# Optimization experiments

Hardware: AMD Instinct MI355X
Metric: run time of the kernel (lower is better)

Reference implementation:

```python
import jax, jax.numpy as jnp
import numpy as np

NUM_CLASSES = 2
IGNORE_INDEX = 0
B, H, W = 4, 512, 512
BIG_I = 2 ** 30  # int sentinel for 'no seed yet'
INF = jnp.float32(1e9)  # distance when a column/image has no seed


def _edt_to_seed(seed):
    """Exact 2D Euclidean distance transform: distance from every pixel to the
    nearest True pixel in `seed` [H, W] (matches scipy distance_transform_edt
    applied to an image whose zeros are `seed`).
    Pass 1: 1D nearest-seed distance down each column via cummax/cummin scans.
    Pass 2: exact lower envelope across rows by brute-force min over k:
            D^2(i,j) = min_k ( (j-k)^2 + g(i,k)^2 ).
    """
    h, w = seed.shape
    rows = jnp.arange(h, dtype=jnp.int32)[:, None]              # [H,1]
    last = jax.lax.cummax(jnp.where(seed, rows, -1), axis=0)     # last seed above
    d_fwd = jnp.where(last >= 0, rows - last, BIG_I)
    nxt = jax.lax.cummin(jnp.where(seed, rows, BIG_I), axis=0, reverse=True)
    d_bwd = jnp.where(nxt < BIG_I, nxt - rows, BIG_I)
    g = jnp.minimum(d_fwd, d_bwd)                                # [H,W] int
    g2 = jnp.where(g >= BIG_I // 2, INF * INF, (g * g).astype(jnp.float32))
    cols = jnp.arange(w, dtype=jnp.float32)
    sq = (cols[:, None] - cols[None, :]) ** 2                    # [Wj,Wk]
    d2 = jnp.min(g2[:, None, :] + sq[None, :, :], axis=-1)       # [H,Wj]
    return jnp.sqrt(d2)


def _distance_map_one(tgt):
    """tgt: [H, W] int labels -> [num_classes, H, W] signed distance maps."""
    maps = []
    for c in range(NUM_CLASSES):
        if c == IGNORE_INDEX:
            maps.append(jnp.zeros(tgt.shape, jnp.float32))
            continue
        mask = tgt == c
        pos_dist = _edt_to_seed(~mask)   # edt(posmask): dist to nearest background
        neg_dist = _edt_to_seed(mask)    # edt(negmask): dist to nearest foreground
        present = jnp.any(mask)          # 'if mask.sum() > 0' guard
        maps.append(jnp.where(present, neg_dist - pos_dist, 0.0))
    return jnp.stack(maps, axis=0)


def setup_inputs() -> dict:
    key = jax.random.key(0)
    k1, k2 = jax.random.split(key)
    pred = jax.random.normal(k1, (B, NUM_CLASSES, H, W), dtype=jnp.float32)
    target = jax.random.randint(k2, (B, H, W), 0, 2, dtype=jnp.int32)
    return {"pred": pred, "target": target}


def reference(pred, target):
    p = jax.nn.softmax(pred, axis=1)                         # [B,C,H,W]
    # sequential over batch to bound the [H,W,W] EDT intermediate
    dmaps = jax.lax.map(_distance_map_one, target)           # [B,C,H,W]
    return jnp.mean(p * dmaps)
```

## Files before the change

kernel.cpp:

```cpp
#include <hip/hip_runtime.h>
#include <math.h>

#define BB 4
#define HH 512
#define WW 512
#define HWSZ (HH * WW)
#define ROWS_BLOCKS 256

#define SK(x) ((x) + ((x) >> 5))


__global__ __launch_bounds__(256) void pack_kernel(
    const int* __restrict__ target,
    unsigned int* __restrict__ cw,
    int* __restrict__ flags)
{
    __shared__ int sCnt;
    int gid = blockIdx.x * 256 + threadIdx.x;
    int b = gid >> 13;
    int rem = gid & 8191;
    int w = rem >> 9;
    int col = rem & 511;

    const int* t = target + b * HWSZ + (w << 5) * WW + col;
    unsigned int word = 0;
#pragma unroll
    for (int i = 0; i < 32; ++i)
        word |= (unsigned int)(t[i * WW] == 1) << i;
    cw[gid] = word;

    int cnt = __popc(word);
#pragma unroll
    for (int off = 32; off > 0; off >>= 1) cnt += __shfl_down(cnt, off, 64);
    if (threadIdx.x == 0) sCnt = 0;
    __syncthreads();
    if ((threadIdx.x & 63) == 0) atomicAdd(&sCnt, cnt);
    __syncthreads();
    if (threadIdx.x == 0) flags[blockIdx.x] = (sCnt > 0);
}

__global__ __launch_bounds__(512) void rows_kernel(
    const unsigned int* __restrict__ cw,
    const float* __restrict__ pred,
    float* __restrict__ partials)
{
    __shared__ unsigned int sW[16 * 512];
    __shared__ float g2n[8][SK(511) + 1], g2p[8][SK(511) + 1];

    int blk = blockIdx.x;
    int b = blk >> 6;
    int g = blk & 63;
    int tid = threadIdx.x;
    int w = tid >> 6, lane = tid & 63;
    int row = 8 * g + w;
    int j0 = 8 * lane;

    const float* p0 = pred + (b * 2 + 0) * HWSZ + row * WW + j0;
    const float* p1 = pred + (b * 2 + 1) * HWSZ + row * WW + j0;
    float4 a0 = *(const float4*)(p0);
    float4 a1 = *(const float4*)(p0 + 4);
    float4 c0 = *(const float4*)(p1);
    float4 c1 = *(const float4*)(p1 + 4);

    const unsigned int* cwb = cw + b * 8192;
#pragma unroll
    for (int t = 0; t < 16; ++t)
        sW[tid + 512 * t] = cwb[tid + 512 * t];
    __syncthreads();

    int wr = row >> 5, bit = row & 31;
    float* G2N = g2n[w];
    float* G2P = g2p[w];
    unsigned int loMask = 0xFFFFFFFFu >> (31 - bit);
    unsigned int hiMask = 0xFFFFFFFFu << bit;
#pragma unroll
    for (int t = 0; t < 8; ++t) {
        int col = lane + (t << 6);
        unsigned int Wr = sW[(wr << 9) + col];
        int dUp, dDn;
        unsigned int m = Wr & loMask;
        if (m) dUp = bit - (31 - __builtin_clz(m));
        else {
            dUp = 0x7FFFFFFF;
            for (int q = wr - 1; q >= 0; --q) {
                unsigned int W = sW[(q << 9) + col];
                if (W) { dUp = row - ((q << 5) + 31 - __builtin_clz(W)); break; }
            }
        }
        m = Wr & hiMask;
        if (m) dDn = __builtin_ctz(m) - bit;
        else {
            dDn = 0x7FFFFFFF;
            for (int q = wr + 1; q < 16; ++q) {
                unsigned int W = sW[(q << 9) + col];
                if (W) { dDn = (q << 5) + __builtin_ctz(W) - row; break; }
            }
        }
        int gN = min(dUp, dDn);
        G2N[SK(col)] = (gN > 511) ? 1e18f : (float)(gN * gN);
        unsigned int Vr = ~Wr;
        m = Vr & loMask;
        if (m) dUp = bit - (31 - __builtin_clz(m));
        else {
            dUp = 0x7FFFFFFF;
            for (int q = wr - 1; q >= 0; --q) {
                unsigned int W = ~sW[(q << 9) + col];
                if (W) { dUp = row - ((q << 5) + 31 - __builtin_clz(W)); break; }
            }
        }
        m = Vr & hiMask;
        if (m) dDn = __builtin_ctz(m) - bit;
        else {
            dDn = 0x7FFFFFFF;
            for (int q = wr + 1; q < 16; ++q) {
                unsigned int W = ~sW[(q << 9) + col];
                if (W) { dDn = (q << 5) + __builtin_ctz(W) - row; break; }
            }
        }
        int gP = min(dUp, dDn);
        G2P[SK(col)] = (gP > 511) ? 1e18f : (float)(gP * gP);
    }

    const float* sel[8];
    float bs[8], sgn[8];
#pragma unroll
    for (int jj = 0; jj < 8; ++jj) {
        float on = G2N[SK(j0 + jj)];
        float op = G2P[SK(j0 + jj)];
        bool fg = (on == 0.0f);
        sel[jj] = fg ? G2P : G2N;
        bs[jj]  = fg ? op : on;
        sgn[jj] = fg ? -1.0f : 1.0f;
    }
    for (int r = 1; r < WW; ++r) {
        float sq = (float)(r * r);
        float mx = 0.0f;
#pragma unroll
        for (int jj = 0; jj < 8; ++jj) mx = fmaxf(mx, bs[jj]);
        if (sq >= mx) break;
#pragma unroll
        for (int jj = 0; jj < 8; ++jj) {
            int kl = j0 + jj - r; kl = kl < 0 ? 0 : kl;
            int kr = j0 + jj + r; kr = kr > (WW - 1) ? (WW - 1) : kr;
            bs[jj] = fminf(bs[jj], sq + sel[jj][SK(kl)]);
            bs[jj] = fminf(bs[jj], sq + sel[jj][SK(kr)]);
        }
    }

    float x0[8] = {a0.x, a0.y, a0.z, a0.w, a1.x, a1.y, a1.z, a1.w};
    float x1[8] = {c0.x, c0.y, c0.z, c0.w, c1.x, c1.y, c1.z, c1.w};
    float acc = 0.0f;
#pragma unroll
    for (int jj = 0; jj < 8; ++jj) {
        float dist = sgn[jj] * sqrtf(bs[jj]);
        float prob = 1.0f / (1.0f + __expf(x0[jj] - x1[jj]));
        acc += prob * dist;
    }
#pragma unroll
    for (int off = 32; off > 0; off >>= 1) acc += __shfl_down(acc, off, 64);
    if (lane == 0) partials[b * HH + row] = acc;
}

__global__ __launch_bounds__(64) void finalize_kernel(
    const int* __restrict__ flags,
    const float* __restrict__ partials,
    float* __restrict__ out)
{
    int k = threadIdx.x;

    double presd[BB];
#pragma unroll
    for (int b = 0; b < BB; ++b) {
        int f = (k < 32) ? flags[b * 32 + k] : 0;
        presd[b] = (__ballot(f != 0) != 0ULL) ? 1.0 : 0.0;
    }

    const float4* p4 = (const float4*)partials;
    double s = 0.0;
#pragma unroll
    for (int t = 0; t < 8; ++t) {
        int v4 = k + 64 * t;
        float4 v = p4[v4];
        double gd = presd[v4 >> 7];
        s += gd * ((double)v.x + (double)v.y + (double)v.z + (double)v.w);
    }
#pragma unroll
    for (int off = 32; off > 0; off >>= 1) s += __shfl_down(s, off, 64);
    if (k == 0)
        out[0] = (float)(s * (1.0 / 2097152.0));
}

extern "C" void kernel_launch(void* const* d_in, const int* in_sizes, int n_in,
                              void* d_out, int out_size, void* d_ws, size_t ws_size,
                              hipStream_t stream) {
    const float* pred = (const float*)d_in[0];
    const int* target = (const int*)d_in[1];
    float* out = (float*)d_out;

    char* ws = (char*)d_ws;
    int* flags = (int*)(ws + 0);
    float* partials = (float*)(ws + 1024);
    unsigned int* cw = (unsigned int*)(ws + 32768);

    pack_kernel<<<128, 256, 0, stream>>>(target, cw, flags);
    rows_kernel<<<ROWS_BLOCKS, 512, 0, stream>>>(cw, pred, partials);
    finalize_kernel<<<1, 64, 0, stream>>>(flags, partials, out);
}
```

Measured before the change: 72.45 us.

## Fuse finalize into rows kernel via atomic last-block reduction; vectorize pack

Drops the separate finalize kernel. Each rows block now reduces its warp sums, atomically adds them into a global double accumulator when its batch has a foreground pixel, and the last block to finish writes the mean. The pack kernel now handles four columns per thread with int4 loads and uint4 stores, using 32 blocks instead of 128. The rows kernel copies the packed words into shared memory as uint4. This removes one launch and the partials round trip, at the cost of global atomics and a summation order that is no longer deterministic.

```diff
diff --git a/kernel.cpp b/kernel.cpp
--- a/kernel.cpp
+++ b/kernel.cpp
@@ -13,23 +13,32 @@
 __global__ __launch_bounds__(256) void pack_kernel(
     const int* __restrict__ target,
     unsigned int* __restrict__ cw,
-    int* __restrict__ flags)
+    int* __restrict__ flags,
+    double* __restrict__ dacc,
+    unsigned int* __restrict__ done)
 {
     __shared__ int sCnt;
-    int gid = blockIdx.x * 256 + threadIdx.x;
-    int b = gid >> 13;
-    int rem = gid & 8191;
-    int w = rem >> 9;
-    int col = rem & 511;
+    int q = blockIdx.x * 256 + threadIdx.x;
+    int b = q >> 11;
+    int rem = q & 2047;
+    int w = rem >> 7;
+    int col = (rem & 127) << 2;
+
+    if (q == 0) { *dacc = 0.0; *done = 0u; }
 
     const int* t = target + b * HWSZ + (w << 5) * WW + col;
-    unsigned int word = 0;
-#pragma unroll
-    for (int i = 0; i < 32; ++i)
-        word |= (unsigned int)(t[i * WW] == 1) << i;
-    cw[gid] = word;
-
-    int cnt = __popc(word);
+    unsigned int w0 = 0, w1 = 0, w2 = 0, w3 = 0;
+#pragma unroll
+    for (int i = 0; i < 32; ++i) {
+        int4 v = *(const int4*)(t + i * WW);
+        w0 |= (unsigned int)(v.x == 1) << i;
+        w1 |= (unsigned int)(v.y == 1) << i;
+        w2 |= (unsigned int)(v.z == 1) << i;
+        w3 |= (unsigned int)(v.w == 1) << i;
+    }
+    ((uint4*)cw)[q] = make_uint4(w0, w1, w2, w3);
+
+    int cnt = __popc(w0) + __popc(w1) + __popc(w2) + __popc(w3);
 #pragma unroll
     for (int off = 32; off > 0; off >>= 1) cnt += __shfl_down(cnt, off, 64);
     if (threadIdx.x == 0) sCnt = 0;
@@ -42,10 +51,15 @@
 __global__ __launch_bounds__(512) void rows_kernel(
     const unsigned int* __restrict__ cw,
     const float* __restrict__ pred,
-    float* __restrict__ partials)
+    const int* __restrict__ flags,
+    double* __restrict__ dacc,
+    unsigned int* __restrict__ done,
+    float* __restrict__ out)
 {
     __shared__ unsigned int sW[16 * 512];
     __shared__ float g2n[8][SK(511) + 1], g2p[8][SK(511) + 1];
+    __shared__ float wsum[8];
+    __shared__ int sPres;
 
     int blk = blockIdx.x;
     int b = blk >> 6;
@@ -62,10 +76,17 @@
     float4 c0 = *(const float4*)(p1);
     float4 c1 = *(const float4*)(p1 + 4);
 
-    const unsigned int* cwb = cw + b * 8192;
-#pragma unroll
-    for (int t = 0; t < 16; ++t)
-        sW[tid + 512 * t] = cwb[tid + 512 * t];
+    if (w == 0) {
+        int f = (lane < 8) ? flags[b * 8 + lane] : 0;
+        unsigned long long blt = __ballot(f != 0);
+        if (lane == 0) sPres = (blt != 0ULL);
+    }
+
+    const uint4* cw4 = (const uint4*)(cw + b * 8192);
+    uint4* sW4 = (uint4*)sW;
+#pragma unroll
+    for (int t = 0; t < 4; ++t)
+        sW4[tid + 512 * t] = cw4[tid + 512 * t];
     __syncthreads();
 
     int wr = row >> 5, bit = row & 31;
@@ -158,36 +179,21 @@
     }
 #pragma unroll
     for (int off = 32; off > 0; off >>= 1) acc += __shfl_down(acc, off, 64);
-    if (lane == 0) partials[b * HH + row] = acc;
-}
-
-__global__ __launch_bounds__(64) void finalize_kernel(
-    const int* __restrict__ flags,
-    const float* __restrict__ partials,
-    float* __restrict__ out)
-{
-    int k = threadIdx.x;
-
-    double presd[BB];
-#pragma unroll
-    for (int b = 0; b < BB; ++b) {
-        int f = (k < 32) ? flags[b * 32 + k] : 0;
-        presd[b] = (__ballot(f != 0) != 0ULL) ? 1.0 : 0.0;
-    }
-
-    const float4* p4 = (const float4*)partials;
-    double s = 0.0;
-#pragma unroll
-    for (int t = 0; t < 8; ++t) {
-        int v4 = k + 64 * t;
-        float4 v = p4[v4];
-        double gd = presd[v4 >> 7];
-        s += gd * ((double)v.x + (double)v.y + (double)v.z + (double)v.w);
-    }
-#pragma unroll
-    for (int off = 32; off > 0; off >>= 1) s += __shfl_down(s, off, 64);
-    if (k == 0)
-        out[0] = (float)(s * (1.0 / 2097152.0));
+
+    if (lane == 0) wsum[w] = acc;
+    __syncthreads();
+    if (tid == 0) {
+        double s = 0.0;
+#pragma unroll
+        for (int i = 0; i < 8; ++i) s += (double)wsum[i];
+        if (sPres) atomicAdd(dacc, s);
+        __threadfence();
+        unsigned int t = atomicAdd(done, 1u);
+        if (t == ROWS_BLOCKS - 1) {
+            double tot = atomicAdd(dacc, 0.0);
+            out[0] = (float)(tot * (1.0 / 2097152.0));
+        }
+    }
 }
 
 extern "C" void kernel_launch(void* const* d_in, const int* in_sizes, int n_in,
@@ -199,10 +205,10 @@
 
     char* ws = (char*)d_ws;
     int* flags = (int*)(ws + 0);
-    float* partials = (float*)(ws + 1024);
+    double* dacc = (double*)(ws + 512);
+    unsigned int* done = (unsigned int*)(ws + 520);
     unsigned int* cw = (unsigned int*)(ws + 32768);
 
-    pack_kernel<<<128, 256, 0, stream>>>(target, cw, flags);
-    rows_kernel<<<ROWS_BLOCKS, 512, 0, stream>>>(cw, pred, partials);
-    finalize_kernel<<<1, 64, 0, stream>>>(flags, partials, out);
+    pack_kernel<<<32, 256, 0, stream>>>(target, cw, flags, dacc, done);
+    rows_kernel<<<ROWS_BLOCKS, 512, 0, stream>>>(cw, pred, flags, dacc, done, out);
 }
```

After: 75.49 us. 4.2% more time.
